# Optimization experiments

Hardware: AMD Instinct MI355X
Metric: run time of the kernel (lower is better)

## Reference

```python
import jax, jax.numpy as jnp
import numpy as np

B, C, H, W = 8, 64, 256, 256

def setup_inputs() -> dict:
    key = jax.random.key(0)
    ks = jax.random.split(key, 8)
    s = 1.0 / np.sqrt(C)
    return {
        "x": jax.random.normal(ks[0], (B, C, H, W), jnp.float32),
        "Wq": jax.random.normal(ks[1], (C, C), jnp.float32) * s,
        "Wk_spe": jax.random.normal(ks[2], (C,), jnp.float32) * s,
        "Wv_spe": jax.random.normal(ks[3], (C, C), jnp.float32) * s,
        "Wv_spa": jax.random.normal(ks[4], (C, C), jnp.float32) * s,
        "Wup": jax.random.normal(ks[5], (C, C), jnp.float32) * s,
        "Wout": jax.random.normal(ks[6], (C, C), jnp.float32) * s,
        "Wnorm": jax.random.normal(ks[7], (1, 1, 7, 7), jnp.float32) * (1.0 / 7.0),
    }

def _forward(x, Wq, Wk_spe, Wv_spe, Wv_spa, Wup, Wout, Wnorm):
    b, c, h, w = x.shape
    # 1x1 convs as channel GEMMs
    q = jnp.einsum('oc,bchw->bohw', Wq, x).reshape(b, c, h * w)      # [B,C,HW]
    v_spe = jnp.einsum('oc,bchw->bohw', Wv_spe, x)                   # [B,C,H,W]
    v_spa = jnp.einsum('oc,bchw->bohw', Wv_spa, x)                   # [B,C,H,W]
    k_spe = jnp.einsum('c,bchw->bhw', Wk_spe, x).reshape(b, h * w)   # [B,HW]
    k_spe = jax.nn.softmax(k_spe, axis=-1)                           # softmax over spatial
    # spectral (channel) attention: pool q with spatial weights
    attn_spe = jnp.einsum('bcn,bn->bc', q, k_spe)                    # [B,C]
    attn_spe = jnp.einsum('oc,bc->bo', Wup, attn_spe)                # conv_up 1x1
    a = jax.nn.softmax(attn_spe, axis=1)                             # softmax over channels
    out_spe = v_spe * a[:, :, None, None]
    # spatial attention: channel-pool q with a
    attn_spa = jnp.einsum('bc,bcn->bn', a, q).reshape(b, 1, h, w)    # [B,1,H,W]
    attn_spa = jax.lax.conv_general_dilated(
        attn_spa, Wnorm, window_strides=(1, 1), padding=((3, 3), (3, 3)),
        dimension_numbers=('NCHW', 'OIHW', 'NCHW'))
    attn_spa = jax.nn.sigmoid(attn_spa)
    out_spa = attn_spa * v_spa
    out = jnp.einsum('oc,bchw->bohw', Wout, out_spa + out_spe)
    return out

def reference(x, Wq, Wk_spe, Wv_spe, Wv_spa, Wup, Wout, Wnorm):
    return _forward(x, Wq, Wk_spe, Wv_spe, Wv_spa, Wup, Wout, Wnorm)
```

## Files before the change

### kernel.cpp

```cpp
#include <hip/hip_runtime.h>
#include <cstdint>
#include <cstddef>

#define Bn 8
#define Cn 64
#define HWn 65536

#define WS_Z 0
#define WS_XPOOL 8
#define WS_A 520
#define WS_WA 1032
#define WS_M1 1544
#define WS_M2 5640
#define WS_S 38408


__global__ __launch_bounds__(256) void k1(const float* __restrict__ x, const float* __restrict__ Wk,
                                          float* __restrict__ ws) {
  __shared__ float e_s[1024];
  __shared__ float red[4];
  int blk = blockIdx.x;
  int b = blk >> 6;
  int base = (blk & 63) << 10;
  int t = threadIdx.x;
  const float* xb = x + (size_t)b * Cn * HWn;
  int n0 = base + t * 4;

  float kx = 0.f, ky = 0.f, kz = 0.f, kw = 0.f;
#pragma unroll 32
  for (int c = 0; c < Cn; ++c) {
    float4 xv = *(const float4*)(xb + (size_t)c * HWn + n0);
    float w = Wk[c];
    kx += w * xv.x; ky += w * xv.y; kz += w * xv.z; kw += w * xv.w;
  }
  float4 ev;
  ev.x = __expf(kx); ev.y = __expf(ky); ev.z = __expf(kz); ev.w = __expf(kw);
  *(float4*)(e_s + t * 4) = ev;
  float part = ev.x + ev.y + ev.z + ev.w;
#pragma unroll
  for (int off = 32; off; off >>= 1) part += __shfl_down(part, off, 64);
  int lane = t & 63, wid = t >> 6;
  if (lane == 0) red[wid] = part;
  __syncthreads();
  if (t == 0) atomicAdd(&ws[WS_Z + b], red[0] + red[1] + red[2] + red[3]);

#pragma unroll 8
  for (int j = 0; j < 16; ++j) {
    int c = wid * 16 + j;
    const float* xc = xb + (size_t)c * HWn + base;
    float acc = 0.f;
#pragma unroll
    for (int rep = 0; rep < 4; ++rep) {
      int idx = rep * 256 + lane * 4;
      float4 xv = *(const float4*)(xc + idx);
      float4 evv = *(const float4*)(e_s + idx);
      acc += xv.x * evv.x + xv.y * evv.y + xv.z * evv.z + xv.w * evv.w;
    }
#pragma unroll
    for (int off = 32; off; off >>= 1) acc += __shfl_down(acc, off, 64);
    if (lane == 0) atomicAdd(&ws[WS_XPOOL + b * Cn + c], acc);
  }
}

__global__ void k2a(const float* __restrict__ Wq, const float* __restrict__ Wup, float* __restrict__ ws) {
  int b = blockIdx.x;
  int t = threadIdx.x;
  __shared__ float xp_s[64], t1[64], a_s[64];
  float Zb = ws[WS_Z + b];
  xp_s[t] = ws[WS_XPOOL + b * 64 + t] / Zb;
  __syncthreads();
  float acc = 0.f;
#pragma unroll
  for (int i = 0; i < 64; ++i) acc += Wq[t * 64 + i] * xp_s[i];
  t1[t] = acc;
  __syncthreads();
  float acc2 = 0.f;
#pragma unroll
  for (int i = 0; i < 64; ++i) acc2 += Wup[t * 64 + i] * t1[i];
  float m = acc2;
#pragma unroll
  for (int off = 32; off; off >>= 1) m = fmaxf(m, __shfl_xor(m, off, 64));
  float e = __expf(acc2 - m);
  float ssum = e;
#pragma unroll
  for (int off = 32; off; off >>= 1) ssum += __shfl_xor(ssum, off, 64);
  float av = e / ssum;
  ws[WS_A + b * 64 + t] = av;
  a_s[t] = av;
  __syncthreads();
  float wav = 0.f;
#pragma unroll
  for (int o = 0; o < 64; ++o) wav += a_s[o] * Wq[o * 64 + t];
  ws[WS_WA + b * 64 + t] = wav;
}

__global__ __launch_bounds__(256) void k2b(const float* __restrict__ Wout, const float* __restrict__ Wv_spa,
                                           const float* __restrict__ Wv_spe, float* __restrict__ ws) {
  __shared__ float A[4096], Bm[4096];
  int j = blockIdx.x;
  for (int idx = threadIdx.x; idx < 4096; idx += 256) {
    A[idx] = Wout[idx];
    if (j == 0)
      Bm[idx] = Wv_spa[idx];
    else
      Bm[idx] = ws[WS_A + (j - 1) * 64 + (idx >> 6)] * Wv_spe[idx];
  }
  __syncthreads();
  float* dst = (j == 0) ? (ws + WS_M1) : (ws + WS_M2 + (size_t)(j - 1) * 4096);
  for (int oi = threadIdx.x; oi < 4096; oi += 256) {
    int o = oi >> 6, i = oi & 63;
    float acc = 0.f;
#pragma unroll
    for (int c = 0; c < 64; ++c) acc += A[o * 64 + c] * Bm[c * 64 + i];
    dst[i * 64 + o] = acc;
  }
}

__global__ __launch_bounds__(256) void k3(const float* __restrict__ x, const float* __restrict__ ws,
                                          float* __restrict__ out) {
  int blk = blockIdx.x;
  int b = blk >> 6;
  int base = (blk & 63) << 10;
  int n0 = base + threadIdx.x * 4;
  const float* xb = x + (size_t)b * Cn * HWn;
  const float* wa = ws + WS_WA + b * 64;
  float kx = 0.f, ky = 0.f, kz = 0.f, kw = 0.f;
#pragma unroll 32
  for (int c = 0; c < Cn; ++c) {
    float4 xv = *(const float4*)(xb + (size_t)c * HWn + n0);
    float w = wa[c];
    kx += w * xv.x; ky += w * xv.y; kz += w * xv.z; kw += w * xv.w;
  }
  float4 r = {kx, ky, kz, kw};
  *(float4*)(out + ((size_t)(b * Cn + 2)) * HWn + n0) = r;
}

__global__ __launch_bounds__(256) void kconv(const float* __restrict__ Wn, const float* __restrict__ out,
                                             float* __restrict__ dst_base, size_t dst_stride) {
  __shared__ float t[38 * 38];
  int blk = blockIdx.x;
  int b = blk >> 6, ty = (blk >> 3) & 7, tx = blk & 7;
  const float* src = out + ((size_t)(b * Cn + 2)) * HWn;
  float* dstp = dst_base + (size_t)b * dst_stride;
  for (int idx = threadIdx.x; idx < 38 * 38; idx += 256) {
    int ly = idx / 38, lx = idx - ly * 38;
    int gy = ty * 32 + ly - 3, gx = tx * 32 + lx - 3;
    float v = 0.f;
    if (gy >= 0 && gy < 256 && gx >= 0 && gx < 256) v = src[gy * 256 + gx];
    t[idx] = v;
  }
  __syncthreads();
#pragma unroll
  for (int q = 0; q < 4; ++q) {
    int pix = threadIdx.x + q * 256;
    int r = pix >> 5, col = pix & 31;
    float acc = 0.f;
#pragma unroll
    for (int dy = 0; dy < 7; ++dy)
#pragma unroll
      for (int dx = 0; dx < 7; ++dx)
        acc += t[(r + dy) * 38 + (col + dx)] * Wn[dy * 7 + dx];
    float sg = 1.f / (1.f + __expf(-acc));
    dstp[(ty * 32 + r) * 256 + tx * 32 + col] = sg;
  }
}

__global__ __launch_bounds__(256, 4) void k4f(const float* __restrict__ x, const float* __restrict__ ws,
                                              float* __restrict__ out) {
  int d = blockIdx.x;
  int xcd = d & 7;
  int j = d >> 3;
  int oc = j & 3;
  int pg = j >> 2;
  int p = pg * 8 + xcd;
  int b = p >> 6;
  int tile = p & 63;
  int t = threadIdx.x;
  const float* m1t = ws + WS_M1 + oc * 16;
  const float* m2t = ws + WS_M2 + (size_t)b * 4096 + oc * 16;

  int n0 = (tile << 10) + t * 4;
  const float* xb = x + (size_t)b * Cn * HWn;
  float4 s4 = *(const float4*)(ws + WS_S + (size_t)b * HWn + n0);
  float4 acc[16];
#pragma unroll
  for (int o = 0; o < 16; ++o) acc[o] = make_float4(0.f, 0.f, 0.f, 0.f);

#pragma unroll 4
  for (int i = 0; i < 64; ++i) {
    float4 xv = *(const float4*)(xb + (size_t)i * HWn + n0);
    float4 sx;
    sx.x = s4.x * xv.x; sx.y = s4.y * xv.y; sx.z = s4.z * xv.z; sx.w = s4.w * xv.w;
    const float* w1r = m1t + i * 64;
    const float* w2r = m2t + i * 64;
#pragma unroll
    for (int o = 0; o < 16; ++o) {
      float w1 = w1r[o], w2 = w2r[o];
      acc[o].x += w1 * sx.x + w2 * xv.x;
      acc[o].y += w1 * sx.y + w2 * xv.y;
      acc[o].z += w1 * sx.z + w2 * xv.z;
      acc[o].w += w1 * sx.w + w2 * xv.w;
    }
  }
  float* op = out + ((size_t)(b * Cn + oc * 16)) * HWn + n0;
#pragma unroll
  for (int o = 0; o < 16; ++o)
    *(float4*)(op + (size_t)o * HWn) = acc[o];
}

#define MSTRIDE 68
__global__ __launch_bounds__(256) void k4m(const float* __restrict__ x, const float* __restrict__ ws,
                                           float* out) {
  __shared__ float M1T[64 * MSTRIDE];
  __shared__ float M2T[64 * MSTRIDE];
  int blk = blockIdx.x;
  int b = blk >> 6;
  int base = (blk & 63) << 10;
  int t = threadIdx.x;
  const float* m1g = ws + WS_M1;
  const float* m2g = ws + WS_M2 + (size_t)b * 4096;
  for (int idx = t; idx < 4096; idx += 256) {
    int c = idx >> 6, o = idx & 63;
    M1T[c * MSTRIDE + o] = m1g[idx];
    M2T[c * MSTRIDE + o] = m2g[idx];
  }
  __syncthreads();
  int n0 = base + t * 4;
  const float* xb = x + (size_t)b * Cn * HWn;
  float* op = out + ((size_t)(b * Cn)) * HWn + n0;
  float4 s4 = *(const float4*)op;
#pragma unroll
  for (int oc = 0; oc < 4; ++oc) {
    float4 acc[16];
#pragma unroll
    for (int o = 0; o < 16; ++o) acc[o] = make_float4(0.f, 0.f, 0.f, 0.f);
    for (int i = 0; i < 64; ++i) {
      float4 xv = *(const float4*)(xb + (size_t)i * HWn + n0);
      float4 sx;
      sx.x = s4.x * xv.x; sx.y = s4.y * xv.y; sx.z = s4.z * xv.z; sx.w = s4.w * xv.w;
      const float* m1r = M1T + i * MSTRIDE + oc * 16;
      const float* m2r = M2T + i * MSTRIDE + oc * 16;
#pragma unroll
      for (int o = 0; o < 16; ++o) {
        float m1 = m1r[o], m2 = m2r[o];
        acc[o].x += m1 * sx.x + m2 * xv.x;
        acc[o].y += m1 * sx.y + m2 * xv.y;
        acc[o].z += m1 * sx.z + m2 * xv.z;
        acc[o].w += m1 * sx.w + m2 * xv.w;
      }
    }
#pragma unroll
    for (int o = 0; o < 16; ++o)
      *(float4*)(op + (size_t)(oc * 16 + o) * HWn) = acc[o];
  }
}

extern "C" void kernel_launch(void* const* d_in, const int* in_sizes, int n_in,
                              void* d_out, int out_size, void* d_ws, size_t ws_size,
                              hipStream_t stream) {
  const float* x      = (const float*)d_in[0];
  const float* Wq     = (const float*)d_in[1];
  const float* Wk     = (const float*)d_in[2];
  const float* Wv_spe = (const float*)d_in[3];
  const float* Wv_spa = (const float*)d_in[4];
  const float* Wup    = (const float*)d_in[5];
  const float* Wout   = (const float*)d_in[6];
  const float* Wn     = (const float*)d_in[7];
  float* out = (float*)d_out;
  float* ws  = (float*)d_ws;

  bool fast = ws_size >= (size_t)(WS_S + Bn * HWn) * sizeof(float);

  (void)hipMemsetAsync(ws, 0, 520 * sizeof(float), stream);
  k1<<<512, 256, 0, stream>>>(x, Wk, ws);
  k2a<<<8, 64, 0, stream>>>(Wq, Wup, ws);
  k2b<<<9, 256, 0, stream>>>(Wout, Wv_spa, Wv_spe, ws);
  k3<<<512, 256, 0, stream>>>(x, ws, out);
  if (fast) {
    kconv<<<512, 256, 0, stream>>>(Wn, out, ws + WS_S, (size_t)HWn);
    k4f<<<2048, 256, 0, stream>>>(x, ws, out);
  } else {
    kconv<<<512, 256, 0, stream>>>(Wn, out, out, (size_t)Cn * HWn);
    k4m<<<512, 256, 0, stream>>>(x, ws, out);
  }
}
```

Before: 426.9 us.

## Keep x tile in registers in k1 to avoid re-reading for pooled sum

```diff
diff --git a/kernel.cpp b/kernel.cpp
--- a/kernel.cpp
+++ b/kernel.cpp
@@ -17,48 +17,43 @@
 
 __global__ __launch_bounds__(256) void k1(const float* __restrict__ x, const float* __restrict__ Wk,
                                           float* __restrict__ ws) {
-  __shared__ float e_s[1024];
-  __shared__ float red[4];
-  int blk = blockIdx.x;
-  int b = blk >> 6;
-  int base = (blk & 63) << 10;
-  int t = threadIdx.x;
-  const float* xb = x + (size_t)b * Cn * HWn;
-  int n0 = base + t * 4;
-
-  float kx = 0.f, ky = 0.f, kz = 0.f, kw = 0.f;
-#pragma unroll 32
+  __shared__ float zred[4];
+  __shared__ float cpart[4][64];
+  int blk = blockIdx.x;
+  int b = blk >> 7;
+  int base = (blk & 127) << 9;
+  int t = threadIdx.x;
+  int lane = t & 63, wid = t >> 6;
+  const float* xb = x + (size_t)b * Cn * HWn;
+  int n0 = base + t * 2;
+
+  float2 xv[64];
+  float kx = 0.f, ky = 0.f;
+#pragma unroll
   for (int c = 0; c < Cn; ++c) {
-    float4 xv = *(const float4*)(xb + (size_t)c * HWn + n0);
+    xv[c] = *(const float2*)(xb + (size_t)c * HWn + n0);
     float w = Wk[c];
-    kx += w * xv.x; ky += w * xv.y; kz += w * xv.z; kw += w * xv.w;
-  }
-  float4 ev;
-  ev.x = __expf(kx); ev.y = __expf(ky); ev.z = __expf(kz); ev.w = __expf(kw);
-  *(float4*)(e_s + t * 4) = ev;
-  float part = ev.x + ev.y + ev.z + ev.w;
+    kx += w * xv[c].x; ky += w * xv[c].y;
+  }
+  float ex = __expf(kx), ey = __expf(ky);
+
+  float part = ex + ey;
 #pragma unroll
   for (int off = 32; off; off >>= 1) part += __shfl_down(part, off, 64);
-  int lane = t & 63, wid = t >> 6;
-  if (lane == 0) red[wid] = part;
-  __syncthreads();
-  if (t == 0) atomicAdd(&ws[WS_Z + b], red[0] + red[1] + red[2] + red[3]);
-
-#pragma unroll 8
-  for (int j = 0; j < 16; ++j) {
-    int c = wid * 16 + j;
-    const float* xc = xb + (size_t)c * HWn + base;
-    float acc = 0.f;
-#pragma unroll
-    for (int rep = 0; rep < 4; ++rep) {
-      int idx = rep * 256 + lane * 4;
-      float4 xv = *(const float4*)(xc + idx);
-      float4 evv = *(const float4*)(e_s + idx);
-      acc += xv.x * evv.x + xv.y * evv.y + xv.z * evv.z + xv.w * evv.w;
-    }
-#pragma unroll
-    for (int off = 32; off; off >>= 1) acc += __shfl_down(acc, off, 64);
-    if (lane == 0) atomicAdd(&ws[WS_XPOOL + b * Cn + c], acc);
+  if (lane == 0) zred[wid] = part;
+
+#pragma unroll
+  for (int c = 0; c < Cn; ++c) {
+    float pc = xv[c].x * ex + xv[c].y * ey;
+#pragma unroll
+    for (int off = 32; off; off >>= 1) pc += __shfl_down(pc, off, 64);
+    if (lane == 0) cpart[wid][c] = pc;
+  }
+  __syncthreads();
+  if (t == 0) atomicAdd(&ws[WS_Z + b], zred[0] + zred[1] + zred[2] + zred[3]);
+  if (t < 64) {
+    float s = cpart[0][t] + cpart[1][t] + cpart[2][t] + cpart[3][t];
+    atomicAdd(&ws[WS_XPOOL + b * 64 + t], s);
   }
 }
 
@@ -272,7 +267,7 @@
   bool fast = ws_size >= (size_t)(WS_S + Bn * HWn) * sizeof(float);
 
   (void)hipMemsetAsync(ws, 0, 520 * sizeof(float), stream);
-  k1<<<512, 256, 0, stream>>>(x, Wk, ws);
+  k1<<<1024, 256, 0, stream>>>(x, Wk, ws);
   k2a<<<8, 64, 0, stream>>>(Wq, Wup, ws);
   k2b<<<9, 256, 0, stream>>>(Wout, Wv_spa, Wv_spe, ws);
   k3<<<512, 256, 0, stream>>>(x, ws, out);
```

Result: faster. 413.5 us (-3.1%).
